# Performance work log

Measured on AMD Instinct MI355X. Metric: run time of the kernel, lower is better.

Reference implementation:

```python
import jax, jax.numpy as jnp
import numpy as np

NUM_HEADS = 16
HEAD_DIM = 128  # d_out / num_heads = 2048 / 16
WINDOW = 2048   # sliding_window_size


def setup_inputs() -> dict:
    key = jax.random.key(0)
    kx, kq, kk, kv, ko = jax.random.split(key, 5)
    b, s, d = 2, 2048, 2048
    scale = 0.02
    return {
        "x": jax.random.normal(kx, (b, s, d), dtype=jnp.float32),
        "Wq": jax.random.normal(kq, (d, d), dtype=jnp.float32) * scale,
        "Wk": jax.random.normal(kk, (d, d), dtype=jnp.float32) * scale,
        "Wv": jax.random.normal(kv, (d, d), dtype=jnp.float32) * scale,
        "Wo": jax.random.normal(ko, (d, d), dtype=jnp.float32) * scale,
    }


def reference(x, Wq, Wk, Wv, Wo):
    b, s, _ = x.shape
    H, Dh, W = NUM_HEADS, HEAD_DIM, WINDOW

    # qkv projections (no bias), split into heads: [b, s, H, Dh]
    q = (x @ Wq).reshape(b, s, H, Dh)
    k = (x @ Wk).reshape(b, s, H, Dh)
    v = (x @ Wv).reshape(b, s, H, Dh)

    # attn scores: [b, H, q, k]
    scores = jnp.einsum("bqhd,bkhd->bhqk", q, k)

    # sliding-window mask from absolute positions (fresh cache: q_start=k_start=0)
    pos = jnp.arange(s)
    diff = pos[:, None] - pos[None, :]  # q_pos - k_pos
    mask = (diff < 0) | (diff >= W)
    scores = jnp.where(mask[None, None], -jnp.inf, scores)

    attn = jax.nn.softmax(scores / np.sqrt(Dh).astype(np.float32), axis=-1)

    # context: [b, s, H, Dh] -> [b, s, d_out]
    ctx = jnp.einsum("bhqk,bkhd->bqhd", attn, v).reshape(b, s, H * Dh)
    return ctx @ Wo
```

## Files before the change

kernel.cpp:

```cpp
#include <hip/hip_runtime.h>

typedef __bf16 bf16;
typedef __bf16 bf16x4 __attribute__((ext_vector_type(4)));
typedef __bf16 bf16x8 __attribute__((ext_vector_type(8)));
typedef float f32x4 __attribute__((ext_vector_type(4)));

#define B_ 2
#define S_ 2048
#define D_ 2048
#define H_ 16
#define DH_ 128
#define QKVN 6144

__device__ __forceinline__ void async_load16(const bf16* g, bf16* l) {
    __builtin_amdgcn_global_load_lds((const __attribute__((address_space(1))) void*)g,
                                     (__attribute__((address_space(3))) void*)l, 16, 0, 0);
}

__device__ __forceinline__ unsigned int bf16_bits(float x) {
    bf16 h = (bf16)x;
    return (unsigned int)__builtin_bit_cast(unsigned short, h);
}

__global__ __launch_bounds__(256) void cvt_kernel(const float* __restrict__ src,
                                                  bf16* __restrict__ dst) {
    size_t i = (size_t)blockIdx.x * 256 + threadIdx.x;
    const float4* s = (const float4*)src;
    float4 a = s[2 * i], b = s[2 * i + 1];
    bf16x8 o;
    o[0] = (bf16)a.x; o[1] = (bf16)a.y; o[2] = (bf16)a.z; o[3] = (bf16)a.w;
    o[4] = (bf16)b.x; o[5] = (bf16)b.y; o[6] = (bf16)b.z; o[7] = (bf16)b.w;
    *(bf16x8*)(dst + 8 * i) = o;
}

__global__ __launch_bounds__(256) void wtrans_kernel(const float* __restrict__ Wq,
                                                     const float* __restrict__ Wk,
                                                     const float* __restrict__ Wv,
                                                     const float* __restrict__ Wo,
                                                     bf16* __restrict__ WqkvT,
                                                     bf16* __restrict__ WoT) {
    __shared__ unsigned int tile[64][65];
    int z = blockIdx.z;
    const float* src = (z == 0) ? Wq : (z == 1) ? Wk : (z == 2) ? Wv : Wo;
    bf16* dst = (z < 3) ? (WqkvT + (size_t)z * D_ * D_) : WoT;
    int r0 = blockIdx.y * 64, c0 = blockIdx.x * 64;
    int t = threadIdx.x;
    int tr = t >> 4, tc4 = (t & 15) * 4;
#pragma unroll
    for (int it = 0; it < 4; ++it) {
        int r = it * 16 + tr;
        float4 v = *(const float4*)(src + (size_t)(r0 + r) * D_ + c0 + tc4);
        tile[r][tc4 + 0] = bf16_bits(v.x);
        tile[r][tc4 + 1] = bf16_bits(v.y);
        tile[r][tc4 + 2] = bf16_bits(v.z);
        tile[r][tc4 + 3] = bf16_bits(v.w);
    }
    __syncthreads();
#pragma unroll
    for (int it = 0; it < 4; ++it) {
        int a = it * 16 + tr;
        unsigned u0 = tile[tc4 + 0][a], u1 = tile[tc4 + 1][a];
        unsigned u2 = tile[tc4 + 2][a], u3 = tile[tc4 + 3][a];
        uint2 v;
        v.x = (u0 & 0xffffu) | (u1 << 16);
        v.y = (u2 & 0xffffu) | (u3 << 16);
        *(uint2*)(dst + (size_t)(c0 + a) * D_ + r0 + tc4) = v;
    }
}

__global__ __launch_bounds__(256) void vtrans_kernel(const bf16* __restrict__ qkv,
                                                     bf16* __restrict__ vt) {
    __shared__ unsigned int tile[64][65];
    int bh = blockIdx.z;
    int b = bh >> 4, h = bh & 15;
    int s0 = blockIdx.x * 64, d0 = blockIdx.y * 64;
    int t = threadIdx.x, tr = t >> 4, tc4 = (t & 15) * 4;
#pragma unroll
    for (int it = 0; it < 4; ++it) {
        int r = it * 16 + tr;
        uint2 v = *(const uint2*)(qkv + (size_t)(b * S_ + s0 + r) * QKVN + 2 * D_ + h * DH_ + d0 + tc4);
        tile[r][tc4 + 0] = v.x & 0xffffu;
        tile[r][tc4 + 1] = v.x >> 16;
        tile[r][tc4 + 2] = v.y & 0xffffu;
        tile[r][tc4 + 3] = v.y >> 16;
    }
    __syncthreads();
#pragma unroll
    for (int it = 0; it < 4; ++it) {
        int a = it * 16 + tr;
        unsigned u0 = tile[tc4 + 0][a], u1 = tile[tc4 + 1][a];
        unsigned u2 = tile[tc4 + 2][a], u3 = tile[tc4 + 3][a];
        uint2 v;
        v.x = (u0 & 0xffffu) | (u1 << 16);
        v.y = (u2 & 0xffffu) | (u3 << 16);
        *(uint2*)(vt + (size_t)bh * DH_ * S_ + (size_t)(d0 + a) * S_ + s0 + tc4) = v;
    }
}

template <typename CT>
__global__ __launch_bounds__(256) void gemm_bt(const bf16* __restrict__ A,
                                               const bf16* __restrict__ Bt,
                                               CT* __restrict__ C,
                                               int M, int N, int K) {
    __shared__ __align__(16) bf16 As[128 * 32];
    __shared__ __align__(16) bf16 Bs[128 * 32];
    int t = threadIdx.x;
    int w = t >> 6, l = t & 63;
    int quad = l >> 4, lr = l & 15;
    int wr = w >> 1, wc = w & 1;
    size_t m0 = (size_t)blockIdx.y * 128, n0 = (size_t)blockIdx.x * 128;
    int srow = l >> 2, scol = (l & 3) * 8;

    f32x4 acc[4][4];
#pragma unroll
    for (int i = 0; i < 4; ++i)
#pragma unroll
        for (int j = 0; j < 4; ++j) acc[i][j] = (f32x4){0.f, 0.f, 0.f, 0.f};

    for (int k0 = 0; k0 < K; k0 += 32) {
        __syncthreads();
#pragma unroll
        for (int i = 0; i < 2; ++i) {
            int c = w * 2 + i;
            async_load16(A + (m0 + c * 16 + srow) * (size_t)K + k0 + scol, As + c * 512);
            async_load16(Bt + (n0 + c * 16 + srow) * (size_t)K + k0 + scol, Bs + c * 512);
        }
        asm volatile("s_waitcnt vmcnt(0)" ::: "memory");
        __syncthreads();
        bf16x8 af[4], bfr[4];
#pragma unroll
        for (int i = 0; i < 4; ++i) af[i] = *(const bf16x8*)(As + (wr * 64 + i * 16 + lr) * 32 + quad * 8);
#pragma unroll
        for (int j = 0; j < 4; ++j) bfr[j] = *(const bf16x8*)(Bs + (wc * 64 + j * 16 + lr) * 32 + quad * 8);
#pragma unroll
        for (int i = 0; i < 4; ++i)
#pragma unroll
            for (int j = 0; j < 4; ++j)
                acc[i][j] = __builtin_amdgcn_mfma_f32_16x16x32_bf16(af[i], bfr[j], acc[i][j], 0, 0, 0);
    }

    size_t bm = m0 + wr * 64 + quad * 4;
    size_t bn = n0 + wc * 64 + lr;
#pragma unroll
    for (int i = 0; i < 4; ++i)
#pragma unroll
        for (int j = 0; j < 4; ++j)
#pragma unroll
            for (int r = 0; r < 4; ++r)
                C[(bm + i * 16 + r) * (size_t)N + bn + j * 16] = (CT)acc[i][j][r];
}

#define QK_K 2048
#define QK_N 6144

__device__ __forceinline__ bf16x8 lds_frag(const bf16* tile, int row, int colByte) {
    int off = row * 128 + (colByte ^ ((row & 7) << 4));
    return *(const bf16x8*)((const char*)tile + off);
}

template <int MH, int NH>
__device__ __forceinline__ void mmaq8(f32x4 (&acc)[8][4], const bf16x8 (&afr)[4][2],
                                      const bf16x8 (&bf)[2][2]) {
    __builtin_amdgcn_s_setprio(1);
#pragma unroll
    for (int i = 0; i < 4; ++i)
#pragma unroll
        for (int j = 0; j < 2; ++j)
#pragma unroll
            for (int kk = 0; kk < 2; ++kk)
                acc[MH * 4 + i][NH * 2 + j] = __builtin_amdgcn_mfma_f32_16x16x32_bf16(
                    afr[i][kk], bf[j][kk], acc[MH * 4 + i][NH * 2 + j], 0, 0, 0);
    __builtin_amdgcn_s_setprio(0);
}

__global__ __launch_bounds__(512, 2) void gemm_qkv(const bf16* __restrict__ A,
                                                   const bf16* __restrict__ Bt,
                                                   bf16* __restrict__ C) {
    __shared__ __align__(16) bf16 As[2][256 * 64];
    __shared__ __align__(16) bf16 Bs[2][256 * 64];

    int t = threadIdx.x;
    int wid = t >> 6, lane = t & 63;
    int quad = lane >> 4, lr = lane & 15;
    int wr = wid >> 2, wn = wid & 3;

    int bid = blockIdx.x;
    int swz = (bid & 7) * 48 + (bid >> 3);
    int tn = swz >> 4, tm = swz & 15;
    size_t m0 = (size_t)tm * 256, n0 = (size_t)tn * 256;

    int row_r[2], c8s_r[2];
#pragma unroll
    for (int r = 0; r < 2; ++r) {
        int idx = r * 512 + t;
        row_r[r] = idx >> 3;
        c8s_r[r] = (idx & 7) ^ (row_r[r] & 7);
    }

    auto stA = [&](int kt, int bufi, int h) {
#pragma unroll
        for (int r = 0; r < 2; ++r)
            async_load16(A + (m0 + h * 128 + row_r[r]) * (size_t)QK_K + kt * 64 + c8s_r[r] * 8,
                         &As[bufi][(h * 1024 + r * 512 + wid * 64) * 8]);
    };
    auto stB = [&](int kt, int bufi, int h) {
#pragma unroll
        for (int r = 0; r < 2; ++r)
            async_load16(Bt + (n0 + h * 128 + row_r[r]) * (size_t)QK_K + kt * 64 + c8s_r[r] * 8,
                         &Bs[bufi][(h * 1024 + r * 512 + wid * 64) * 8]);
    };

    f32x4 acc[8][4];
#pragma unroll
    for (int i = 0; i < 8; ++i)
#pragma unroll
        for (int j = 0; j < 4; ++j) acc[i][j] = (f32x4){0.f, 0.f, 0.f, 0.f};

    bf16x8 afr[4][2], bf0[2][2], bf1[2][2];

    auto readA = [&](int bufi, int mh) {
#pragma unroll
        for (int i = 0; i < 4; ++i)
#pragma unroll
            for (int kk = 0; kk < 2; ++kk)
                afr[i][kk] = lds_frag(As[bufi], mh * 128 + wr * 64 + i * 16 + lr, kk * 64 + quad * 16);
    };
    auto readB = [&](int bufi, int nh, bf16x8 (&bf)[2][2]) {
#pragma unroll
        for (int j = 0; j < 2; ++j)
#pragma unroll
            for (int kk = 0; kk < 2; ++kk)
                bf[j][kk] = lds_frag(Bs[bufi], nh * 128 + wn * 32 + j * 16 + lr, kk * 64 + quad * 16);
    };

    stA(0, 0, 0);
    stB(0, 0, 0);
    stB(0, 0, 1);
    stA(0, 0, 1);
    asm volatile("s_waitcnt vmcnt(4)" ::: "memory");
    __builtin_amdgcn_s_barrier();

    const int NKT = QK_K / 64;
    for (int kt = 0; kt < NKT - 1; ++kt) {
        int cb = kt & 1, nb = cb ^ 1;
        readA(cb, 0);
        readB(cb, 0, bf0);
        stA(kt + 1, nb, 0);
        asm volatile("s_waitcnt vmcnt(4)" ::: "memory");
        __builtin_amdgcn_s_barrier();
        asm volatile("s_waitcnt lgkmcnt(0)" ::: "memory");
        __builtin_amdgcn_sched_barrier(0);
        mmaq8<0, 0>(acc, afr, bf0);
        __builtin_amdgcn_s_barrier();
        readB(cb, 1, bf1);
        stB(kt + 1, nb, 0);
        asm volatile("s_waitcnt vmcnt(4)" ::: "memory");
        __builtin_amdgcn_s_barrier();
        asm volatile("s_waitcnt lgkmcnt(0)" ::: "memory");
        __builtin_amdgcn_sched_barrier(0);
        mmaq8<0, 1>(acc, afr, bf1);
        __builtin_amdgcn_s_barrier();
        readA(cb, 1);
        stB(kt + 1, nb, 1);
        __builtin_amdgcn_s_barrier();
        asm volatile("s_waitcnt lgkmcnt(0)" ::: "memory");
        __builtin_amdgcn_sched_barrier(0);
        mmaq8<1, 0>(acc, afr, bf0);
        __builtin_amdgcn_s_barrier();
        stA(kt + 1, nb, 1);
        asm volatile("s_waitcnt vmcnt(4)" ::: "memory");
        __builtin_amdgcn_s_barrier();
        mmaq8<1, 1>(acc, afr, bf1);
        __builtin_amdgcn_s_barrier();
    }

    {
        int cb = (NKT - 1) & 1;
        readA(cb, 0);
        readB(cb, 0, bf0);
        asm volatile("s_waitcnt vmcnt(2)" ::: "memory");
        __builtin_amdgcn_s_barrier();
        asm volatile("s_waitcnt lgkmcnt(0)" ::: "memory");
        __builtin_amdgcn_sched_barrier(0);
        mmaq8<0, 0>(acc, afr, bf0);
        __builtin_amdgcn_s_barrier();
        readB(cb, 1, bf1);
        asm volatile("s_waitcnt vmcnt(0)" ::: "memory");
        __builtin_amdgcn_s_barrier();
        asm volatile("s_waitcnt lgkmcnt(0)" ::: "memory");
        __builtin_amdgcn_sched_barrier(0);
        mmaq8<0, 1>(acc, afr, bf1);
        __builtin_amdgcn_s_barrier();
        readA(cb, 1);
        __builtin_amdgcn_s_barrier();
        asm volatile("s_waitcnt lgkmcnt(0)" ::: "memory");
        __builtin_amdgcn_sched_barrier(0);
        mmaq8<1, 0>(acc, afr, bf0);
        __builtin_amdgcn_s_barrier();
        mmaq8<1, 1>(acc, afr, bf1);
    }

#pragma unroll
    for (int mh = 0; mh < 2; ++mh)
#pragma unroll
        for (int i = 0; i < 4; ++i)
#pragma unroll
            for (int nh = 0; nh < 2; ++nh)
#pragma unroll
                for (int j = 0; j < 2; ++j)
#pragma unroll
                    for (int r = 0; r < 4; ++r) {
                        size_t row = m0 + mh * 128 + wr * 64 + i * 16 + quad * 4 + r;
                        size_t col = n0 + nh * 128 + wn * 32 + j * 16 + lr;
                        C[row * QK_N + col] = (bf16)acc[mh * 4 + i][nh * 2 + j][r];
                    }
}

__global__ __launch_bounds__(128) void attn_kernel(const bf16* __restrict__ qkv,
                                                   const bf16* __restrict__ vt,
                                                   bf16* __restrict__ ctx) {
    __shared__ __align__(16) bf16 Ks[2][64 * 128];
    __shared__ __align__(16) bf16 Vts[2][128 * 64];
    __shared__ __align__(16) bf16 Ps[2][32][68];

    int y = blockIdx.y;
    int p = blockIdx.x;
    int b = y >> 4, h = y & 15;
    int t = threadIdx.x, w = t >> 6, l = t & 63;
    int quad = l >> 4, lr = l & 15;

    const bf16* qbase = qkv + (size_t)b * S_ * QKVN + h * DH_;
    const bf16* kbase = qbase + D_;
    const bf16* vbase = vt + (size_t)y * DH_ * S_;

    const int qtA = p, qtB = 31 - p;
    const int nA = p + 1;

    auto stage = [&](int kt, int bi) {
#pragma unroll
        for (int ii = 0; ii < 8; ++ii) {
            int i = 8 * w + ii;
            int row = 4 * i + (l >> 4);
            int cl = (l & 15) ^ (row & 7);
            async_load16(kbase + (size_t)(kt * 64 + row) * QKVN + cl * 8, Ks[bi] + i * 512);
        }
#pragma unroll
        for (int ii = 0; ii < 8; ++ii) {
            int i = 8 * w + ii;
            int dh = 8 * i + (l >> 3);
            int cl = (l & 7) ^ (dh & 7);
            async_load16(vbase + (size_t)dh * S_ + kt * 64 + cl * 8, Vts[bi] + i * 512);
        }
    };

    const float sc2 = 0.12751745f;

    int qt = qtA, q0 = qt * 64;
    bf16x8 qf[2][4];
    auto loadQ = [&]() {
#pragma unroll
        for (int g = 0; g < 2; ++g)
#pragma unroll
            for (int kk = 0; kk < 4; ++kk) {
                bf16x8 raw = *(const bf16x8*)(qbase + (size_t)(q0 + w * 32 + g * 16 + lr) * QKVN + kk * 32 + quad * 8);
#pragma unroll
                for (int e = 0; e < 8; ++e) qf[g][kk][e] = (bf16)((float)raw[e] * sc2);
            }
    };
    loadQ();

    float L_r[2][4];
    f32x4 o[2][8];
#pragma unroll
    for (int g = 0; g < 2; ++g) {
#pragma unroll
        for (int r = 0; r < 4; ++r) L_r[g][r] = 0.f;
#pragma unroll
        for (int nt = 0; nt < 8; ++nt) o[g][nt] = (f32x4){0.f, 0.f, 0.f, 0.f};
    }

    auto epilogue = [&](int q0e) {
#pragma unroll
        for (int g = 0; g < 2; ++g) {
#pragma unroll
            for (int d = 1; d < 16; d <<= 1)
#pragma unroll
                for (int r = 0; r < 4; ++r) L_r[g][r] += __shfl_xor(L_r[g][r], d, 64);
#pragma unroll
            for (int r = 0; r < 4; ++r) {
                float inv = __builtin_amdgcn_rcpf(L_r[g][r]);
                int q = q0e + w * 32 + g * 16 + quad * 4 + r;
#pragma unroll
                for (int nt = 0; nt < 8; ++nt)
                    ctx[(size_t)(b * S_ + q) * D_ + h * DH_ + nt * 16 + lr] = (bf16)(o[g][nt][r] * inv);
            }
        }
    };

    stage(0, 0);

    for (int it = 0; it < 33; ++it) {
        int buf = it & 1;
        asm volatile("s_waitcnt vmcnt(0)" ::: "memory");
        __syncthreads();
        if (it + 1 < 33) {
            int nit = it + 1;
            int nkt = (nit < nA) ? nit : (nit - nA);
            stage(nkt, buf ^ 1);
        }
        int kt = (it < nA) ? it : (it - nA);

        f32x4 s[2][4];
#pragma unroll
        for (int g = 0; g < 2; ++g)
#pragma unroll
            for (int jt = 0; jt < 4; ++jt) s[g][jt] = (f32x4){0.f, 0.f, 0.f, 0.f};
#pragma unroll
        for (int kk = 0; kk < 4; ++kk)
#pragma unroll
            for (int jt = 0; jt < 4; ++jt) {
                bf16x8 kf = *(const bf16x8*)(Ks[buf] + (jt * 16 + lr) * 128 + ((4 * kk + quad) ^ (lr & 7)) * 8);
                s[0][jt] = __builtin_amdgcn_mfma_f32_16x16x32_bf16(qf[0][kk], kf, s[0][jt], 0, 0, 0);
                s[1][jt] = __builtin_amdgcn_mfma_f32_16x16x32_bf16(qf[1][kk], kf, s[1][jt], 0, 0, 0);
            }

        bool diag = (kt == qt);
#pragma unroll
        for (int g = 0; g < 2; ++g) {
#pragma unroll
            for (int jt = 0; jt < 4; ++jt) {
                int keyi = jt * 16 + lr;
#pragma unroll
                for (int r = 0; r < 4; ++r) {
                    float s2 = s[g][jt][r];
                    if (diag && keyi > w * 32 + g * 16 + quad * 4 + r) s2 = -3.0e38f;
                    float pv = __builtin_amdgcn_exp2f(s2);
                    s[g][jt][r] = pv;
                    L_r[g][r] += pv;
                }
            }
#pragma unroll
            for (int jt = 0; jt < 4; ++jt)
#pragma unroll
                for (int r = 0; r < 4; ++r)
                    Ps[w][g * 16 + quad * 4 + r][jt * 16 + lr] = (bf16)s[g][jt][r];
        }
        asm volatile("s_waitcnt lgkmcnt(0)" ::: "memory");

#pragma unroll
        for (int ks = 0; ks < 2; ++ks) {
            bf16x8 pf[2];
#pragma unroll
            for (int g = 0; g < 2; ++g) {
                const bf16* pp = &Ps[w][g * 16 + lr][ks * 32 + quad * 8];
                bf16x4 lo = *(const bf16x4*)pp;
                bf16x4 hi = *(const bf16x4*)(pp + 4);
                pf[g] = __builtin_shufflevector(lo, hi, 0, 1, 2, 3, 4, 5, 6, 7);
            }
#pragma unroll
            for (int nt = 0; nt < 8; ++nt) {
                bf16x8 vf = *(const bf16x8*)(Vts[buf] + (nt * 16 + lr) * 64 + ((4 * ks + quad) ^ (lr & 7)) * 8);
                o[0][nt] = __builtin_amdgcn_mfma_f32_16x16x32_bf16(pf[0], vf, o[0][nt], 0, 0, 0);
                o[1][nt] = __builtin_amdgcn_mfma_f32_16x16x32_bf16(pf[1], vf, o[1][nt], 0, 0, 0);
            }
        }

        if (it == nA - 1) {
            epilogue(q0);
            qt = qtB;
            q0 = qt * 64;
            loadQ();
#pragma unroll
            for (int g = 0; g < 2; ++g) {
#pragma unroll
                for (int r = 0; r < 4; ++r) L_r[g][r] = 0.f;
#pragma unroll
                for (int nt = 0; nt < 8; ++nt) o[g][nt] = (f32x4){0.f, 0.f, 0.f, 0.f};
            }
        }
    }

    epilogue(q0);
}

extern "C" void kernel_launch(void* const* d_in, const int* in_sizes, int n_in,
                              void* d_out, int out_size, void* d_ws, size_t ws_size,
                              hipStream_t stream) {
    const float* x  = (const float*)d_in[0];
    const float* Wq = (const float*)d_in[1];
    const float* Wk = (const float*)d_in[2];
    const float* Wv = (const float*)d_in[3];
    const float* Wo = (const float*)d_in[4];
    float* out = (float*)d_out;

    char* ws = (char*)d_ws;
    bf16* WqkvT = (bf16*)(ws);
    bf16* WoT   = (bf16*)(ws + 25165824);
    bf16* qkv   = (bf16*)(ws + 33554432);
    bf16* vt    = (bf16*)(ws + 83886080);
    bf16* ctx   = (bf16*)(ws + 100663296);
    bf16* xb    = (bf16*)(ws + 117440512);

    cvt_kernel<<<4096, 256, 0, stream>>>(x, xb);
    wtrans_kernel<<<dim3(32, 32, 4), 256, 0, stream>>>(Wq, Wk, Wv, Wo, WqkvT, WoT);
    gemm_qkv<<<dim3(384), 512, 0, stream>>>(xb, WqkvT, qkv);
    vtrans_kernel<<<dim3(32, 2, 32), 256, 0, stream>>>(qkv, vt);
    attn_kernel<<<dim3(16, 32), 128, 0, stream>>>(qkv, vt, ctx);
    gemm_bt<float><<<dim3(16, 32), 256, 0, stream>>>(ctx, WoT, out, B_ * S_, D_, D_);
}
```

Baseline: 417.1 us.

## Deepen QKV GEMM prefetch pipeline with unrolled two-stage ping-pong loop

Restructures the QKV projection GEMM main loop so global-to-LDS loads run further ahead, prefetching most of the next tile's halves before the current tile is consumed. The loop is unrolled by two with fixed buffer indices and looser vmcnt waits (6 instead of 4), keeping more loads in flight. The goal is to hide global memory latency behind the MFMA work. It hardcodes the K-tile count (32) and adds a long special-cased epilogue, which increases code size and the chance of ordering mistakes.

```diff
diff --git a/kernel.cpp b/kernel.cpp
--- a/kernel.cpp
+++ b/kernel.cpp
@@ -233,70 +233,108 @@
                 bf[j][kk] = lds_frag(Bs[bufi], nh * 128 + wn * 32 + j * 16 + lr, kk * 64 + quad * 16);
     };
 
-    stA(0, 0, 0);
-    stB(0, 0, 0);
-    stB(0, 0, 1);
-    stA(0, 0, 1);
+    stA(0, 0, 0); stB(0, 0, 0); stB(0, 0, 1); stA(0, 0, 1);
     asm volatile("s_waitcnt vmcnt(4)" ::: "memory");
+    stA(1, 1, 0); stB(1, 1, 0); stB(1, 1, 1);
+    asm volatile("s_waitcnt vmcnt(6)" ::: "memory");
     __builtin_amdgcn_s_barrier();
 
-    const int NKT = QK_K / 64;
-    for (int kt = 0; kt < NKT - 1; ++kt) {
-        int cb = kt & 1, nb = cb ^ 1;
-        readA(cb, 0);
-        readB(cb, 0, bf0);
-        stA(kt + 1, nb, 0);
-        asm volatile("s_waitcnt vmcnt(4)" ::: "memory");
+    for (int it2 = 0; it2 < 15; ++it2) {
+        int tt = 2 * it2;
+        readA(0, 0);
+        readB(0, 0, bf0);
+        stA(tt + 1, 1, 1);
         __builtin_amdgcn_s_barrier();
         asm volatile("s_waitcnt lgkmcnt(0)" ::: "memory");
         __builtin_amdgcn_sched_barrier(0);
         mmaq8<0, 0>(acc, afr, bf0);
         __builtin_amdgcn_s_barrier();
-        readB(cb, 1, bf1);
-        stB(kt + 1, nb, 0);
-        asm volatile("s_waitcnt vmcnt(4)" ::: "memory");
+        readB(0, 1, bf1);
+        stA(tt + 2, 0, 0);
         __builtin_amdgcn_s_barrier();
         asm volatile("s_waitcnt lgkmcnt(0)" ::: "memory");
         __builtin_amdgcn_sched_barrier(0);
         mmaq8<0, 1>(acc, afr, bf1);
         __builtin_amdgcn_s_barrier();
-        readA(cb, 1);
-        stB(kt + 1, nb, 1);
+        readA(0, 1);
+        stB(tt + 2, 0, 0);
         __builtin_amdgcn_s_barrier();
         asm volatile("s_waitcnt lgkmcnt(0)" ::: "memory");
         __builtin_amdgcn_sched_barrier(0);
         mmaq8<1, 0>(acc, afr, bf0);
         __builtin_amdgcn_s_barrier();
-        stA(kt + 1, nb, 1);
-        asm volatile("s_waitcnt vmcnt(4)" ::: "memory");
+        stB(tt + 2, 0, 1);
+        asm volatile("s_waitcnt vmcnt(6)" ::: "memory");
         __builtin_amdgcn_s_barrier();
         mmaq8<1, 1>(acc, afr, bf1);
         __builtin_amdgcn_s_barrier();
+        readA(1, 0);
+        readB(1, 0, bf0);
+        stA(tt + 2, 0, 1);
+        __builtin_amdgcn_s_barrier();
+        asm volatile("s_waitcnt lgkmcnt(0)" ::: "memory");
+        __builtin_amdgcn_sched_barrier(0);
+        mmaq8<0, 0>(acc, afr, bf0);
+        __builtin_amdgcn_s_barrier();
+        readB(1, 1, bf1);
+        stA(tt + 3, 1, 0);
+        __builtin_amdgcn_s_barrier();
+        asm volatile("s_waitcnt lgkmcnt(0)" ::: "memory");
+        __builtin_amdgcn_sched_barrier(0);
+        mmaq8<0, 1>(acc, afr, bf1);
+        __builtin_amdgcn_s_barrier();
+        readA(1, 1);
+        stB(tt + 3, 1, 0);
+        __builtin_amdgcn_s_barrier();
+        asm volatile("s_waitcnt lgkmcnt(0)" ::: "memory");
+        __builtin_amdgcn_sched_barrier(0);
+        mmaq8<1, 0>(acc, afr, bf0);
+        __builtin_amdgcn_s_barrier();
+        stB(tt + 3, 1, 1);
+        asm volatile("s_waitcnt vmcnt(6)" ::: "memory");
+        __builtin_amdgcn_s_barrier();
+        mmaq8<1, 1>(acc, afr, bf1);
+        __builtin_amdgcn_s_barrier();
     }
 
     {
-        int cb = (NKT - 1) & 1;
-        readA(cb, 0);
-        readB(cb, 0, bf0);
-        asm volatile("s_waitcnt vmcnt(2)" ::: "memory");
+        readA(0, 0);
+        readB(0, 0, bf0);
+        stA(31, 1, 1);
         __builtin_amdgcn_s_barrier();
         asm volatile("s_waitcnt lgkmcnt(0)" ::: "memory");
         __builtin_amdgcn_sched_barrier(0);
         mmaq8<0, 0>(acc, afr, bf0);
         __builtin_amdgcn_s_barrier();
-        readB(cb, 1, bf1);
+        readB(0, 1, bf1);
+        __builtin_amdgcn_s_barrier();
+        asm volatile("s_waitcnt lgkmcnt(0)" ::: "memory");
+        __builtin_amdgcn_sched_barrier(0);
+        mmaq8<0, 1>(acc, afr, bf1);
+        __builtin_amdgcn_s_barrier();
+        readA(0, 1);
+        __builtin_amdgcn_s_barrier();
+        asm volatile("s_waitcnt lgkmcnt(0)" ::: "memory");
+        __builtin_amdgcn_sched_barrier(0);
+        mmaq8<1, 0>(acc, afr, bf0);
+        __builtin_amdgcn_s_barrier();
         asm volatile("s_waitcnt vmcnt(0)" ::: "memory");
         __builtin_amdgcn_s_barrier();
+        mmaq8<1, 1>(acc, afr, bf1);
+        __builtin_amdgcn_s_barrier();
+        readA(1, 0);
+        readB(1, 0, bf0);
+        asm volatile("s_waitcnt lgkmcnt(0)" ::: "memory");
+        __builtin_amdgcn_sched_barrier(0);
+        mmaq8<0, 0>(acc, afr, bf0);
+        readB(1, 1, bf1);
         asm volatile("s_waitcnt lgkmcnt(0)" ::: "memory");
         __builtin_amdgcn_sched_barrier(0);
         mmaq8<0, 1>(acc, afr, bf1);
-        __builtin_amdgcn_s_barrier();
-        readA(cb, 1);
-        __builtin_amdgcn_s_barrier();
+        readA(1, 1);
         asm volatile("s_waitcnt lgkmcnt(0)" ::: "memory");
         __builtin_amdgcn_sched_barrier(0);
         mmaq8<1, 0>(acc, afr, bf0);
-        __builtin_amdgcn_s_barrier();
         mmaq8<1, 1>(acc, afr, bf1);
     }
 
```

Result: no change. 411.8 us (-1.3%).
